# Performance work log

Measured on AMD Instinct MI355X. Metric: run time of the kernel, lower is better.

Reference implementation:

```python
import jax, jax.numpy as jnp
import numpy as np

P = 16          # patch size
D = 256         # embed dim (complex channels)
L = 2           # depth (num blocks)
NE = 4          # num experts
FF = 1024       # ffn hidden = expand * D
B, T, C, IH, IW = 1, 8, 4, 256, 256
HP, WP = IH // P, IW // P


def setup_inputs():
    key = jax.random.key(0)
    ks = iter(jax.random.split(key, 40))
    r = lambda shape, s=0.02: jax.random.normal(next(ks), shape, jnp.float32) * s
    sD = 1.0 / np.sqrt(D)
    return {
        'x': jax.random.normal(next(ks), (B, T, C, IH, IW), jnp.float32),
        'dt': jax.random.uniform(next(ks), (B, T), jnp.float32, 0.1, 1.0),
        'Wenc': r((C * P * P, 2 * D)),
        'benc': jnp.zeros((2 * D,), jnp.float32),
        'Wdec': r((2 * D, C * P * P)),
        'bdec': jnp.zeros((C * P * P,), jnp.float32),
        'ln_sp_w': jnp.ones((L, 2 * D), jnp.float32),
        'ln_sp_b': jnp.zeros((L, 2 * D), jnp.float32),
        'conv_w': r((L, 2 * D, 2 * D, 3, 3)),
        'conv_b': jnp.zeros((L, 2 * D), jnp.float32),
        'E_re': r((L, D, D), sD), 'E_im': r((L, D, D), sD),
        'Ed_re': r((L, D, D), sD), 'Ed_im': r((L, D, D), sD),
        'Ws_re': r((L, D, D), sD), 'Ws_im': r((L, D, D), sD),
        'Wg': r((L, 2 * D, D)),
        'bg': jnp.zeros((L, D), jnp.float32),
        'lam_re': r((L, D), 1.0), 'lam_im': r((L, D), 1.0),
        'ln_t_w': jnp.ones((L, 2 * D), jnp.float32),
        'ln_t_b': jnp.zeros((L, 2 * D), jnp.float32),
        'Wr': r((L, 2 * D, NE)),
        'W1': r((L, NE, 2 * D, FF)),
        'W2': r((L, NE, FF, 2 * D)),
    }


def _ln(x, w, b):
    m = x.mean(-1, keepdims=True)
    v = ((x - m) ** 2).mean(-1, keepdims=True)
    return (x - m) * jax.lax.rsqrt(v + 1e-5) * w + b


def _block(z, h_prev, flux_prev, dt, bp):
    (ln_sp_w, ln_sp_b, conv_w, conv_b, E_re, E_im, Ed_re, Ed_im,
     Ws_re, Ws_im, Wg, bg, lam_re, lam_im, ln_t_w, ln_t_b, Wr, W1, W2) = bp
    Bq, Tq, Dq, H, W = z.shape
    # --- spatial process: LN + conv on concat(real, imag), complex residual ---
    zf = z.reshape(Bq * Tq, Dq, H, W)
    zr = jnp.concatenate([zf.real, zf.imag], axis=1)
    zn = _ln(zr.transpose(0, 2, 3, 1), ln_sp_w, ln_sp_b).transpose(0, 3, 1, 2)
    zs = jax.lax.conv_general_dilated(zn, conv_w, (1, 1), 'SAME',
                                      dimension_numbers=('NCHW', 'OIHW', 'NCHW'))
    zs = zs + conv_b[None, :, None, None]
    re, im = jnp.split(zs, 2, axis=1)
    x = (zf + (re + 1j * im)).reshape(Bq, Tq, Dq, H, W)
    # --- eigen-basis encode ---
    Eb = E_re + 1j * E_im
    x_eigen = jnp.einsum('btdhw,de->bthwe', x, Eb)   # [B,T,H,W,D] complex
    x_mean = x_eigen.mean(axis=(2, 3))               # [B,T,D] complex
    # --- sequential gated flux recurrence over T ---
    Ws = Ws_re + 1j * Ws_im
    def step(flux, xm):
        source = xm @ Ws
        feat = jnp.concatenate([xm.real, xm.imag], -1)
        gate = jax.nn.sigmoid(feat @ Wg + bg)        # real [B,D]
        new_flux = gate * flux + (1.0 - gate) * source
        return new_flux, (new_flux, source, gate)
    _, (flux_seq, source_seq, gate_seq) = jax.lax.scan(step, flux_prev, x_mean.transpose(1, 0, 2))
    flux_seq = flux_seq.transpose(1, 0, 2)
    source_seq = source_seq.transpose(1, 0, 2)
    gate_seq = gate_seq.transpose(1, 0, 2)
    g = gate_seq[:, :, None, None, :]
    forcing = x_eigen * g + source_seq[:, :, None, None, :] * (1.0 - g)
    # --- transition operators ---
    lam = -(jax.nn.softplus(lam_re) + 1e-2) + 1j * lam_im        # [D]
    op_decay = jnp.exp(lam[None, None, :] * dt[:, :, None])      # [B,T,D] complex
    op_forcing = (op_decay - 1.0) / lam
    a = jnp.broadcast_to(op_decay[:, :, None, None, :], forcing.shape)
    u = forcing * op_forcing[:, :, None, None, :]
    # --- parallel linear scan h_t = a_t * h_{t-1} + u_t along T ---
    def comb(c1, c2):
        a1, u1 = c1
        a2, u2 = c2
        return a1 * a2, u1 * a2 + u2
    _, h = jax.lax.associative_scan(comb, (a, u), axis=1)
    # as written in source: h_prev contribution is h_prev * op_decay at every t
    h = h + h_prev.reshape(Bq, 1, H, W, Dq) * a
    last_h = h[:, -1].reshape(Bq * H * W, 1, Dq)
    last_flux = flux_seq[:, -1]
    # --- eigen decode + temporal LN + MoE FFN ---
    Ed = Ed_re + 1j * Ed_im
    x_out = jnp.einsum('bthwe,ed->btdhw', h, Ed)
    xf = x_out.reshape(Bq * Tq, Dq, H, W)
    xr = jnp.concatenate([xf.real, xf.imag], axis=1)
    xn = _ln(xr.transpose(0, 2, 3, 1), ln_t_w, ln_t_b)           # [BT,H,W,2D]
    tok = xn.reshape(-1, 2 * Dq)
    probs = jax.nn.softmax(tok @ Wr, axis=-1)                    # [N,E]
    hid = jax.nn.gelu(jnp.einsum('nd,edf->nef', tok, W1))
    y = jnp.einsum('nef,efd,ne->nd', hid, W2, probs)             # [N,2D]
    xc = xn[..., :Dq] + 1j * xn[..., Dq:]
    delta = (y[..., :Dq] + 1j * y[..., Dq:]).reshape(Bq * Tq, H, W, Dq)
    x_cplx = (xc + delta).reshape(Bq, Tq, H, W, Dq).transpose(0, 1, 4, 2, 3)
    return x + x_cplx, last_h, last_flux


def _forward(x, dt, Wenc, benc, Wdec, bdec, ln_sp_w, ln_sp_b, conv_w, conv_b,
             E_re, E_im, Ed_re, Ed_im, Ws_re, Ws_im, Wg, bg, lam_re, lam_im,
             ln_t_w, ln_t_b, Wr, W1, W2):
    # encoder: patchify + linear -> complex latent [B,T,D,HP,WP]
    xp = x.reshape(B, T, C, HP, P, WP, P).transpose(0, 1, 3, 5, 2, 4, 6)
    xp = xp.reshape(B, T, HP, WP, C * P * P)
    ze = xp @ Wenc + benc                                        # [B,T,HP,WP,2D]
    z = (ze[..., :D] + 1j * ze[..., D:]).transpose(0, 1, 4, 2, 3)
    h_prev = jnp.zeros((B * HP * WP, 1, D), jnp.complex64)
    flux_prev = jnp.zeros((B, D), jnp.complex64)
    bparams = (ln_sp_w, ln_sp_b, conv_w, conv_b, E_re, E_im, Ed_re, Ed_im,
               Ws_re, Ws_im, Wg, bg, lam_re, lam_im, ln_t_w, ln_t_b, Wr, W1, W2)
    for i in range(L):
        bp = tuple(p[i] for p in bparams)
        z, h_prev, flux_prev = _block(z, h_prev, flux_prev, dt, bp)
    # decoder: linear + unpatchify (real output)
    zr = jnp.concatenate([z.real, z.imag], axis=2).transpose(0, 1, 3, 4, 2)
    yo = zr @ Wdec + bdec                                        # [B,T,HP,WP,C*P*P]
    out = yo.reshape(B, T, HP, WP, C, P, P).transpose(0, 1, 4, 2, 5, 3, 6)
    return out.reshape(B, T, C, IH, IW)


def reference(x, dt, Wenc, benc, Wdec, bdec, ln_sp_w, ln_sp_b, conv_w, conv_b,
              E_re, E_im, Ed_re, Ed_im, Ws_re, Ws_im, Wg, bg, lam_re, lam_im,
              ln_t_w, ln_t_b, Wr, W1, W2):
    return _forward(x, dt, Wenc, benc, Wdec, bdec, ln_sp_w, ln_sp_b, conv_w, conv_b,
                    E_re, E_im, Ed_re, Ed_im, Ws_re, Ws_im, Wg, bg, lam_re, lam_im,
                    ln_t_w, ln_t_b, Wr, W1, W2)
```

## Files before the change

### kernel.cpp

```cpp
#include <hip/hip_runtime.h>
#include <hip/hip_bf16.h>


#define TOKS 2048

typedef __bf16 bf16;
typedef __attribute__((ext_vector_type(8))) __bf16 bf16x8;
typedef __attribute__((ext_vector_type(4))) __bf16 bf16x4;
typedef __attribute__((ext_vector_type(4))) float f32x4;

enum GMode { EENC = 0, ECONV, ESQ, EMOE1, EMOE2, EDEC };

template <int MODE>
__global__ __launch_bounds__(256) void mgemm_k(
    const bf16* __restrict__ A, const bf16* __restrict__ Bt,
    const float* __restrict__ bias, float* __restrict__ C, int K, int N) {
  __shared__ __align__(16) bf16 As[64 * 40];
  __shared__ __align__(16) bf16 Bs[64 * 40];
  const int tid = threadIdx.x;
  const int bm = blockIdx.x * 64, bn = blockIdx.y * 64;
  const int lane = tid & 63, w = tid >> 6;
  const int wm = (w & 1) * 32, wn = (w >> 1) * 32;
  const int quad = lane >> 4, l16 = lane & 15;
  const int srow = tid >> 2, sko = (tid & 3) << 3;

  f32x4 acc[2][2] = {};
  const int kiter = K / 32;

  auto loadA = [&](int kt) -> bf16x8 {
    return *(const bf16x8*)&A[(size_t)(bm + srow) * K + kt * 32 + sko];
  };
  auto loadB = [&](int kt) -> bf16x8 {
    return *(const bf16x8*)&Bt[(size_t)(bn + srow) * K + kt * 32 + sko];
  };

  bf16x8 pa = loadA(0), pb = loadB(0);
  for (int kt = 0; kt < kiter; kt++) {
    *(bf16x8*)&As[srow * 40 + sko] = pa;
    *(bf16x8*)&Bs[srow * 40 + sko] = pb;
    __syncthreads();
    if (kt + 1 < kiter) {
      pa = loadA(kt + 1);
      pb = loadB(kt + 1);
    }
    const bf16x8 a0 = *(const bf16x8*)&As[(wm + l16) * 40 + quad * 8];
    const bf16x8 a1 = *(const bf16x8*)&As[(wm + 16 + l16) * 40 + quad * 8];
    const bf16x8 b0 = *(const bf16x8*)&Bs[(wn + l16) * 40 + quad * 8];
    const bf16x8 b1 = *(const bf16x8*)&Bs[(wn + 16 + l16) * 40 + quad * 8];
    acc[0][0] = __builtin_amdgcn_mfma_f32_16x16x32_bf16(a0, b0, acc[0][0], 0, 0, 0);
    acc[0][1] = __builtin_amdgcn_mfma_f32_16x16x32_bf16(a0, b1, acc[0][1], 0, 0, 0);
    acc[1][0] = __builtin_amdgcn_mfma_f32_16x16x32_bf16(a1, b0, acc[1][0], 0, 0, 0);
    acc[1][1] = __builtin_amdgcn_mfma_f32_16x16x32_bf16(a1, b1, acc[1][1], 0, 0, 0);
    __syncthreads();
  }

#pragma unroll
  for (int i = 0; i < 2; i++) {
#pragma unroll
    for (int j = 0; j < 2; j++) {
#pragma unroll
      for (int r = 0; r < 4; r++) {
        const int gm = bm + wm + i * 16 + quad * 4 + r;
        const int gn = bn + wn + j * 16 + l16;
        const float v = acc[i][j][r];
        if constexpr (MODE == EENC) {
          C[(size_t)gm * 512 + gn] = v + bias[gn];
        } else if constexpr (MODE == ESQ) {
          C[(size_t)gm * 512 + gn] = v;
        } else {
          const int t = gm >> 8, hp = (gm >> 4) & 15, wp = gm & 15;
          const int c = gn >> 8, ph = (gn >> 4) & 15, pw = gn & 15;
          C[(size_t)(((t * 4 + c) * 256 + hp * 16 + ph) << 8) + wp * 16 + pw] =
              v + bias[gn];
        }
      }
    }
  }
}

template <int MODE, int SPLIT>
__global__ __launch_bounds__(256) void mgemm2_k(
    const bf16* __restrict__ A, const bf16* __restrict__ Bt,
    const float* __restrict__ scalev, bf16* __restrict__ C16,
    float* __restrict__ Cpart, int K, int N) {
  __shared__ __align__(16) bf16 As[128 * 40];
  __shared__ __align__(16) bf16 Bs[128 * 40];
  const int tid = threadIdx.x;
  const int bm = blockIdx.x * 128, bn = blockIdx.y * 128;
  const int lane = tid & 63, w = tid >> 6;
  const int wm = (w & 1) * 64, wn = (w >> 1) * 64;
  const int quad = lane >> 4, l16 = lane & 15;
  const int srow = tid >> 1, sko = (tid & 1) << 4;

  const int kbase = (SPLIT > 1) ? blockIdx.z * (K / SPLIT) : 0;
  const int kiter = K / (32 * SPLIT);
  if constexpr (MODE == EMOE1) Bt += (size_t)blockIdx.z * 524288;

  f32x4 acc[4][4] = {};

  int cv_t = 0, cv_h = 0, cv_w = 0;
  if constexpr (MODE == ECONV) {
    const int gm = bm + srow;
    cv_t = gm >> 8;
    cv_h = (gm >> 4) & 15;
    cv_w = gm & 15;
  }

  auto loadA = [&](int kt, int half) -> bf16x8 {
    const int gk = kbase + kt * 32 + sko + half * 8;
    if constexpr (MODE == ECONV) {
      const int s = gk >> 9, ci = gk & 511;
      const int kh = s / 3, kw = s - kh * 3;
      const int hh = cv_h + kh - 1, ww = cv_w + kw - 1;
      if (hh >= 0 && hh < 16 && ww >= 0 && ww < 16)
        return *(const bf16x8*)&A[(size_t)(((cv_t << 8) + hh * 16 + ww) << 9) +
                                  ci];
      bf16x8 zz;
#pragma unroll
      for (int q = 0; q < 8; q++) zz[q] = (bf16)0.0f;
      return zz;
    } else {
      return *(const bf16x8*)&A[(size_t)(bm + srow) * K + gk];
    }
  };
  auto loadB = [&](int kt, int half) -> bf16x8 {
    return *(const bf16x8*)&Bt[(size_t)(bn + srow) * K + kbase + kt * 32 + sko +
                               half * 8];
  };

  bf16x8 pa0 = loadA(0, 0), pa1 = loadA(0, 1);
  bf16x8 pb0 = loadB(0, 0), pb1 = loadB(0, 1);
  for (int kt = 0; kt < kiter; kt++) {
    *(bf16x8*)&As[srow * 40 + sko] = pa0;
    *(bf16x8*)&As[srow * 40 + sko + 8] = pa1;
    *(bf16x8*)&Bs[srow * 40 + sko] = pb0;
    *(bf16x8*)&Bs[srow * 40 + sko + 8] = pb1;
    __syncthreads();
    if (kt + 1 < kiter) {
      pa0 = loadA(kt + 1, 0);
      pa1 = loadA(kt + 1, 1);
      pb0 = loadB(kt + 1, 0);
      pb1 = loadB(kt + 1, 1);
    }
    bf16x8 af[4], bfr[4];
#pragma unroll
    for (int i = 0; i < 4; i++)
      af[i] = *(const bf16x8*)&As[(wm + i * 16 + l16) * 40 + quad * 8];
#pragma unroll
    for (int j = 0; j < 4; j++)
      bfr[j] = *(const bf16x8*)&Bs[(wn + j * 16 + l16) * 40 + quad * 8];
#pragma unroll
    for (int i = 0; i < 4; i++)
#pragma unroll
      for (int j = 0; j < 4; j++)
        acc[i][j] =
            __builtin_amdgcn_mfma_f32_16x16x32_bf16(af[i], bfr[j], acc[i][j], 0, 0, 0);
    __syncthreads();
  }

#pragma unroll
  for (int i = 0; i < 4; i++) {
#pragma unroll
    for (int j = 0; j < 4; j++) {
#pragma unroll
      for (int r = 0; r < 4; r++) {
        const int gm = bm + wm + i * 16 + quad * 4 + r;
        const int gn = bn + wn + j * 16 + l16;
        const float v = acc[i][j][r];
        if constexpr (SPLIT > 1) {
          Cpart[(size_t)blockIdx.z * 1048576 + (size_t)gm * 512 + gn] = v;
        } else {
          const float t = 0.7978845608028654f * (v + 0.044715f * v * v * v);
          const float g = 0.5f * v * (1.f + tanhf(t));
          const float p = scalev[gm * 4 + blockIdx.z];
          C16[(size_t)gm * 4096 + blockIdx.z * 1024 + gn] = (bf16)(p * g);
        }
      }
    }
  }
}

__global__ __launch_bounds__(256) void conv_ep_k(
    const float* __restrict__ parts, const float* __restrict__ bias,
    const float* __restrict__ resid, float* __restrict__ xb,
    bf16* __restrict__ xb16) {
  const int i4 = (blockIdx.x * 256 + threadIdx.x) << 2;
  const int c = i4 & 511;
  const float4 p0 = *(const float4*)&parts[i4];
  const float4 p1 = *(const float4*)&parts[1048576 + i4];
  const float4 p2 = *(const float4*)&parts[2097152 + i4];
  const float4 p3 = *(const float4*)&parts[3145728 + i4];
  const float4 bi = *(const float4*)&bias[c];
  const float4 rz = *(const float4*)&resid[i4];
  float4 o;
  o.x = p0.x + p1.x + p2.x + p3.x + bi.x + rz.x;
  o.y = p0.y + p1.y + p2.y + p3.y + bi.y + rz.y;
  o.z = p0.z + p1.z + p2.z + p3.z + bi.z + rz.z;
  o.w = p0.w + p1.w + p2.w + p3.w + bi.w + rz.w;
  *(float4*)&xb[i4] = o;
  bf16x4 o16 = {(bf16)o.x, (bf16)o.y, (bf16)o.z, (bf16)o.w};
  *(bf16x4*)&xb16[i4] = o16;
}

__global__ __launch_bounds__(256) void addf_k(const float* __restrict__ xb,
                                              const float* __restrict__ zn,
                                              const float* __restrict__ parts,
                                              float* __restrict__ z,
                                              bf16* __restrict__ z16) {
  const int i4 = (blockIdx.x * 256 + threadIdx.x) << 2;
  const float4 a = *(const float4*)&xb[i4];
  const float4 b = *(const float4*)&zn[i4];
  const float4 p0 = *(const float4*)&parts[i4];
  const float4 p1 = *(const float4*)&parts[1048576 + i4];
  const float4 p2 = *(const float4*)&parts[2097152 + i4];
  const float4 p3 = *(const float4*)&parts[3145728 + i4];
  float4 o;
  o.x = a.x + b.x + p0.x + p1.x + p2.x + p3.x;
  o.y = a.y + b.y + p0.y + p1.y + p2.y + p3.y;
  o.z = a.z + b.z + p0.z + p1.z + p2.z + p3.z;
  o.w = a.w + b.w + p0.w + p1.w + p2.w + p3.w;
  *(float4*)&z[i4] = o;
  bf16x4 o16 = {(bf16)o.x, (bf16)o.y, (bf16)o.z, (bf16)o.w};
  *(bf16x4*)&z16[i4] = o16;
}

template <bool DO_PROBS>
__global__ __launch_bounds__(256) void ln_k(
    const float* __restrict__ in, const float* __restrict__ w,
    const float* __restrict__ b, const float* __restrict__ Wr,
    float* __restrict__ out, bf16* __restrict__ out16,
    float* __restrict__ probs) {
  const int wv = threadIdx.x >> 6, lane = threadIdx.x & 63;
  const int n = (blockIdx.x << 2) + wv;
  const float* row = in + (size_t)n * 512;
  float v[8];
  float s = 0.f, s2 = 0.f;
#pragma unroll
  for (int i = 0; i < 8; i++) {
    const float x = row[(i << 6) + lane];
    v[i] = x;
    s += x;
    s2 += x * x;
  }
#pragma unroll
  for (int off = 32; off > 0; off >>= 1) {
    s += __shfl_down(s, off);
    s2 += __shfl_down(s2, off);
  }
  s = __shfl(s, 0);
  s2 = __shfl(s2, 0);
  const float m = s * (1.f / 512.f);
  const float var = s2 * (1.f / 512.f) - m * m;
  const float r = rsqrtf(var + 1e-5f);
  float a0 = 0.f, a1 = 0.f, a2 = 0.f, a3 = 0.f;
#pragma unroll
  for (int i = 0; i < 8; i++) {
    const int c = (i << 6) + lane;
    const float o = (v[i] - m) * r * w[c] + b[c];
    out[(size_t)n * 512 + c] = o;
    out16[(size_t)n * 512 + c] = (bf16)o;
    if constexpr (DO_PROBS) {
      a0 += o * Wr[c * 4 + 0];
      a1 += o * Wr[c * 4 + 1];
      a2 += o * Wr[c * 4 + 2];
      a3 += o * Wr[c * 4 + 3];
    }
  }
  if constexpr (DO_PROBS) {
#pragma unroll
    for (int off = 32; off > 0; off >>= 1) {
      a0 += __shfl_down(a0, off);
      a1 += __shfl_down(a1, off);
      a2 += __shfl_down(a2, off);
      a3 += __shfl_down(a3, off);
    }
    if (lane == 0) {
      const float mx = fmaxf(fmaxf(a0, a1), fmaxf(a2, a3));
      const float e0 = expf(a0 - mx), e1 = expf(a1 - mx), e2 = expf(a2 - mx),
                  e3 = expf(a3 - mx);
      const float inv = 1.f / (e0 + e1 + e2 + e3);
      probs[n * 4 + 0] = e0 * inv;
      probs[n * 4 + 1] = e1 * inv;
      probs[n * 4 + 2] = e2 * inv;
      probs[n * 4 + 3] = e3 * inv;
    }
  }
}

__global__ __launch_bounds__(256) void cvt_all_k(
    const float* __restrict__ x, const float* __restrict__ Wenc,
    const float* __restrict__ Wdec, const float* __restrict__ W1,
    const float* __restrict__ W2, const float* __restrict__ E_re,
    const float* __restrict__ E_im, const float* __restrict__ Ed_re,
    const float* __restrict__ Ed_im, const float* __restrict__ conv_w,
    bf16* __restrict__ Ae, bf16* __restrict__ WencT, bf16* __restrict__ WdecT,
    bf16* __restrict__ W1T, bf16* __restrict__ W2Tc, bf16* __restrict__ MEt,
    bf16* __restrict__ convBt) {
  __shared__ float tile[32][33];
  const int tid = threadIdx.x;
  int b = blockIdx.x;
  const int tx = tid & 31, ty = tid >> 5;
  auto tpose = [&](const float* src, bf16* dst, int K, int N, int dstride,
                   int k0, int n0) {
#pragma unroll
    for (int r = 0; r < 4; r++)
      tile[ty + 8 * r][tx] = src[(size_t)(k0 + ty + 8 * r) * N + n0 + tx];
    __syncthreads();
#pragma unroll
    for (int r = 0; r < 4; r++)
      dst[(size_t)(n0 + ty + 8 * r) * dstride + k0 + tx] =
          (bf16)tile[tx][ty + 8 * r];
  };
  if (b < 1024) {
    const int id = b * 256 + tid;
    const int n = id >> 7;
    const int kc = (id & 127) << 3;
    const int t = n >> 8, hp = (n >> 4) & 15, wp = n & 15;
    const int c = kc >> 8, ph = (kc >> 4) & 15, pw = kc & 15;
    const float* src =
        &x[(size_t)(((t * 4 + c) * 256 + hp * 16 + ph) << 8) + wp * 16 + pw];
    const float4 v0 = *(const float4*)src;
    const float4 v1 = *(const float4*)(src + 4);
    bf16* d = &Ae[(size_t)n * 1024 + kc];
    d[0] = (bf16)v0.x; d[1] = (bf16)v0.y; d[2] = (bf16)v0.z; d[3] = (bf16)v0.w;
    d[4] = (bf16)v1.x; d[5] = (bf16)v1.y; d[6] = (bf16)v1.z; d[7] = (bf16)v1.w;
    return;
  }
  b -= 1024;
  if (b < 512) {
    tpose(Wenc, WencT, 1024, 512, 1024, (b & 31) * 32, (b >> 5) * 32);
    return;
  }
  b -= 512;
  if (b < 512) {
    tpose(Wdec, WdecT, 512, 1024, 512, (b & 15) * 32, (b >> 4) * 32);
    return;
  }
  b -= 512;
  if (b < 4096) {
    const int z = b >> 9, rem = b & 511;
    tpose(W1 + (size_t)z * 524288, W1T + (size_t)z * 524288, 512, 1024, 512,
          (rem & 15) * 32, (rem >> 4) * 32);
    return;
  }
  b -= 4096;
  if (b < 4096) {
    const int z = b >> 9, rem = b & 511;
    const int l = z >> 2, e = z & 3;
    tpose(W2 + (size_t)z * 524288, W2Tc + (size_t)l * 2097152 + e * 1024, 1024,
          512, 4096, (rem & 31) * 32, (rem >> 5) * 32);
    return;
  }
  b -= 4096;
  if (b < 4096) {
    const int z = b >> 10;
    const int l = z >> 1, which = z & 1;
    const float* Er = (which ? Ed_re : E_re) + l * 65536;
    const float* Ei = (which ? Ed_im : E_im) + l * 65536;
    bf16* dst = MEt + (size_t)z * 262144;
    const int idx = (b & 1023) * 256 + tid;
    const int j = idx >> 9, k = idx & 511;
    const int kk = k & 255, jj = j & 255;
    const float er = Er[kk * 256 + jj], ei = Ei[kk * 256 + jj];
    const float v = (k < 256) ? ((j < 256) ? er : ei) : ((j < 256) ? -ei : er);
    dst[idx] = (bf16)v;
    return;
  }
  b -= 4096;
  {
    const int z = b / 2304;
    const int rem = b - z * 2304;
    const float* src = conv_w + (size_t)z * 2359296;
    bf16* d = convBt + (size_t)z * 2359296;
    const int idx = (rem * 256 + tid) << 2;
    const int co = idx / 4608;
    const int r2 = idx - co * 4608;
    const int s = r2 >> 9, ci = r2 & 511;
    bf16x4 o;
#pragma unroll
    for (int q = 0; q < 4; q++)
      o[q] = (bf16)src[(size_t)(co * 512 + ci + q) * 9 + s];
    *(bf16x4*)&d[idx] = o;
  }
}

__global__ __launch_bounds__(256) void srcgate_k(
    const float* __restrict__ xe, const float* __restrict__ Wsr,
    const float* __restrict__ Wsi, const float* __restrict__ Wg,
    const float* __restrict__ bg, float* __restrict__ srcs,
    float* __restrict__ gts) {
  const int t = blockIdx.x, part = blockIdx.y, d = threadIdx.x;
  __shared__ float sxm[512];
  for (int c = d; c < 512; c += 256) {
    const float* col = xe + (size_t)(t << 8) * 512 + c;
    float s0 = 0.f, s1 = 0.f, s2 = 0.f, s3 = 0.f;
    for (int p = 0; p < 256; p += 4) {
      s0 += col[(size_t)(p + 0) * 512];
      s1 += col[(size_t)(p + 1) * 512];
      s2 += col[(size_t)(p + 2) * 512];
      s3 += col[(size_t)(p + 3) * 512];
    }
    sxm[c] = ((s0 + s1) + (s2 + s3)) * (1.f / 256.f);
  }
  __syncthreads();
  if (part == 0) {
    float s0 = 0.f, s1 = 0.f, s2 = 0.f, s3 = 0.f;
#pragma unroll 4
    for (int e = 0; e < 256; e += 4) {
      s0 += sxm[e + 0] * Wsr[(e + 0) * 256 + d] - sxm[256 + e + 0] * Wsi[(e + 0) * 256 + d];
      s1 += sxm[e + 1] * Wsr[(e + 1) * 256 + d] - sxm[256 + e + 1] * Wsi[(e + 1) * 256 + d];
      s2 += sxm[e + 2] * Wsr[(e + 2) * 256 + d] - sxm[256 + e + 2] * Wsi[(e + 2) * 256 + d];
      s3 += sxm[e + 3] * Wsr[(e + 3) * 256 + d] - sxm[256 + e + 3] * Wsi[(e + 3) * 256 + d];
    }
    srcs[t * 512 + d] = (s0 + s1) + (s2 + s3);
  } else if (part == 1) {
    float s0 = 0.f, s1 = 0.f, s2 = 0.f, s3 = 0.f;
#pragma unroll 4
    for (int e = 0; e < 256; e += 4) {
      s0 += sxm[e + 0] * Wsi[(e + 0) * 256 + d] + sxm[256 + e + 0] * Wsr[(e + 0) * 256 + d];
      s1 += sxm[e + 1] * Wsi[(e + 1) * 256 + d] + sxm[256 + e + 1] * Wsr[(e + 1) * 256 + d];
      s2 += sxm[e + 2] * Wsi[(e + 2) * 256 + d] + sxm[256 + e + 2] * Wsr[(e + 2) * 256 + d];
      s3 += sxm[e + 3] * Wsi[(e + 3) * 256 + d] + sxm[256 + e + 3] * Wsr[(e + 3) * 256 + d];
    }
    srcs[t * 512 + 256 + d] = (s0 + s1) + (s2 + s3);
  } else {
    float s0 = 0.f, s1 = 0.f, s2 = 0.f, s3 = 0.f;
#pragma unroll 4
    for (int c = 0; c < 512; c += 4) {
      s0 += sxm[c + 0] * Wg[(c + 0) * 256 + d];
      s1 += sxm[c + 1] * Wg[(c + 1) * 256 + d];
      s2 += sxm[c + 2] * Wg[(c + 2) * 256 + d];
      s3 += sxm[c + 3] * Wg[(c + 3) * 256 + d];
    }
    const float ga = (s0 + s1) + (s2 + s3) + bg[d];
    gts[t * 256 + d] = 1.f / (1.f + expf(-ga));
  }
}

template <bool FIRST>
__global__ __launch_bounds__(256) void time_scan_k(
    const float* __restrict__ xe, const float* __restrict__ gts,
    const float* __restrict__ srcs, const float* __restrict__ lamre,
    const float* __restrict__ lamim, const float* __restrict__ dt,
    bf16* __restrict__ hout16, float* __restrict__ hprev) {
  const int d = threadIdx.x;
  const int p = blockIdx.x;
  const float lr0 = lamre[d];
  const float sp = (lr0 > 20.f) ? lr0 : log1pf(expf(lr0));
  const float lre = -(sp + 0.01f);
  const float lim = lamim[d];
  const float den = lre * lre + lim * lim;
  float ar[8], ai[8], ofr[8], ofi[8];
#pragma unroll
  for (int t = 0; t < 8; t++) {
    const float dtv = dt[t];
    const float er = expf(lre * dtv);
    const float odr = er * cosf(lim * dtv);
    const float odi = er * sinf(lim * dtv);
    ar[t] = odr;
    ai[t] = odi;
    const float nr = odr - 1.f, ni = odi;
    ofr[t] = (nr * lre + ni * lim) / den;
    ofi[t] = (ni * lre - nr * lim) / den;
  }
  float hr = 0.f, hi = 0.f;
  float hpr = 0.f, hpi = 0.f;
  if constexpr (!FIRST) {
    hpr = hprev[p * 512 + d];
    hpi = hprev[p * 512 + 256 + d];
  }
  float o7r = 0.f, o7i = 0.f;
#pragma unroll
  for (int t = 0; t < 8; t++) {
    const size_t base = (size_t)((t << 8) + p) * 512;
    const float xr = xe[base + d], xi = xe[base + 256 + d];
    const float g = gts[t * 256 + d];
    const float sr = srcs[t * 512 + d], si = srcs[t * 512 + 256 + d];
    const float fr = xr * g + sr * (1.f - g);
    const float fi = xi * g + si * (1.f - g);
    const float ur = fr * ofr[t] - fi * ofi[t];
    const float ui = fr * ofi[t] + fi * ofr[t];
    const float nhr = ur + ar[t] * hr - ai[t] * hi;
    const float nhi = ui + ar[t] * hi + ai[t] * hr;
    hr = nhr;
    hi = nhi;
    const float outr = hr + ar[t] * hpr - ai[t] * hpi;
    const float outi = hi + ar[t] * hpi + ai[t] * hpr;
    hout16[base + d] = (bf16)outr;
    hout16[base + 256 + d] = (bf16)outi;
    if (t == 7) {
      o7r = outr;
      o7i = outi;
    }
  }
  hprev[p * 512 + d] = o7r;
  hprev[p * 512 + 256 + d] = o7i;
}

extern "C" void kernel_launch(void* const* d_in, const int* in_sizes, int n_in,
                              void* d_out, int out_size, void* d_ws,
                              size_t ws_size, hipStream_t stream) {
  const float* x_in = (const float*)d_in[0];
  const float* dt = (const float*)d_in[1];
  const float* Wenc = (const float*)d_in[2];
  const float* benc = (const float*)d_in[3];
  const float* Wdec = (const float*)d_in[4];
  const float* bdec = (const float*)d_in[5];
  const float* ln_sp_w = (const float*)d_in[6];
  const float* ln_sp_b = (const float*)d_in[7];
  const float* conv_w = (const float*)d_in[8];
  const float* conv_b = (const float*)d_in[9];
  const float* E_re = (const float*)d_in[10];
  const float* E_im = (const float*)d_in[11];
  const float* Ed_re = (const float*)d_in[12];
  const float* Ed_im = (const float*)d_in[13];
  const float* Ws_re = (const float*)d_in[14];
  const float* Ws_im = (const float*)d_in[15];
  const float* Wg = (const float*)d_in[16];
  const float* bg = (const float*)d_in[17];
  const float* lam_re = (const float*)d_in[18];
  const float* lam_im = (const float*)d_in[19];
  const float* ln_t_w = (const float*)d_in[20];
  const float* ln_t_b = (const float*)d_in[21];
  const float* Wr = (const float*)d_in[22];
  const float* W1 = (const float*)d_in[23];
  const float* W2 = (const float*)d_in[24];
  float* out = (float*)d_out;

  float* ws = (float*)d_ws;
  size_t off = 0;
  auto allocf = [&](size_t n) {
    float* p = ws + off;
    off += n;
    return p;
  };
  auto allocb = [&](size_t n) {
    bf16* p = (bf16*)(ws + off);
    off += n / 2;
    return p;
  };
  float* z = allocf((size_t)TOKS * 512);
  float* zn = allocf((size_t)TOKS * 512);
  float* xb = allocf((size_t)TOKS * 512);
  float* xe = allocf((size_t)TOKS * 512);
  float* parts = allocf((size_t)4 * TOKS * 512);
  float* hprev = allocf(256 * 512);
  float* srcs = allocf(8 * 512);
  float* gts = allocf(8 * 256);
  float* probs = allocf((size_t)TOKS * 4);
  bf16* zn16 = allocb((size_t)TOKS * 512);
  bf16* xb16 = allocb((size_t)TOKS * 512);
  bf16* z16 = allocb((size_t)TOKS * 512);
  bf16* hb16 = allocb((size_t)TOKS * 512);
  bf16* hid16 = allocb((size_t)TOKS * 4096);
  bf16* Aenc16 = allocb((size_t)TOKS * 1024);
  bf16* WencT = allocb((size_t)512 * 1024);
  bf16* WdecT = allocb((size_t)1024 * 512);
  bf16* MEt = allocb((size_t)4 * 512 * 512);
  bf16* convBt = allocb((size_t)2 * 512 * 4608);
  bf16* W1T = allocb((size_t)8 * 1024 * 512);
  bf16* W2Tc = allocb((size_t)2 * 512 * 4096);

  cvt_all_k<<<18944, 256, 0, stream>>>(x_in, Wenc, Wdec, W1, W2, E_re, E_im,
                                       Ed_re, Ed_im, conv_w, Aenc16, WencT,
                                       WdecT, W1T, W2Tc, MEt, convBt);

  mgemm_k<EENC><<<dim3(32, 8), 256, 0, stream>>>(Aenc16, WencT, benc, z, 1024,
                                                 512);

  for (int l = 0; l < 2; l++) {
    ln_k<false><<<512, 256, 0, stream>>>(z, ln_sp_w + l * 512,
                                         ln_sp_b + l * 512, nullptr, zn, zn16,
                                         nullptr);
    mgemm2_k<ECONV, 4><<<dim3(16, 4, 4), 256, 0, stream>>>(
        zn16, convBt + (size_t)l * 512 * 4608, nullptr, nullptr, parts, 4608,
        512);
    conv_ep_k<<<1024, 256, 0, stream>>>(parts, conv_b + l * 512, z, xb, xb16);
    mgemm_k<ESQ><<<dim3(32, 8), 256, 0, stream>>>(
        xb16, MEt + (size_t)(l * 2) * 262144, nullptr, xe, 512, 512);
    srcgate_k<<<dim3(8, 3), 256, 0, stream>>>(xe, Ws_re + l * 65536,
                                              Ws_im + l * 65536,
                                              Wg + l * 131072, bg + l * 256,
                                              srcs, gts);
    if (l == 0)
      time_scan_k<true><<<256, 256, 0, stream>>>(
          xe, gts, srcs, lam_re, lam_im, dt, hb16, hprev);
    else
      time_scan_k<false><<<256, 256, 0, stream>>>(
          xe, gts, srcs, lam_re + 256, lam_im + 256, dt, hb16, hprev);
    mgemm_k<ESQ><<<dim3(32, 8), 256, 0, stream>>>(
        hb16, MEt + (size_t)(l * 2 + 1) * 262144, nullptr, xe, 512, 512);
    ln_k<true><<<512, 256, 0, stream>>>(xe, ln_t_w + l * 512, ln_t_b + l * 512,
                                        Wr + l * 2048, zn, zn16, probs);
    mgemm2_k<EMOE1, 1><<<dim3(16, 8, 4), 256, 0, stream>>>(
        zn16, W1T + (size_t)l * 2097152, probs, hid16, nullptr, 512, 1024);
    mgemm2_k<EMOE2, 4><<<dim3(16, 4, 4), 256, 0, stream>>>(
        hid16, W2Tc + (size_t)l * 2097152, nullptr, nullptr, parts, 4096, 512);
    addf_k<<<1024, 256, 0, stream>>>(xb, zn, parts, z, z16);
  }

  mgemm_k<EDEC><<<dim3(32, 16), 256, 0, stream>>>(z16, WdecT, bdec, out, 512,
                                                  1024);
}
```

Baseline: 495.1 us.

## Unify GEMMs on 64x64 tiles, split-K small GEMMs, fuse LN into combine kernels

```diff
diff --git a/kernel.cpp b/kernel.cpp
--- a/kernel.cpp
+++ b/kernel.cpp
@@ -3,6 +3,7 @@
 
 
 #define TOKS 2048
+#define PSLICE 1048576
 
 typedef __bf16 bf16;
 typedef __attribute__((ext_vector_type(8))) __bf16 bf16x8;
@@ -11,10 +12,12 @@
 
 enum GMode { EENC = 0, ECONV, ESQ, EMOE1, EMOE2, EDEC };
 
-template <int MODE>
+template <int MODE, int SPLIT>
 __global__ __launch_bounds__(256) void mgemm_k(
     const bf16* __restrict__ A, const bf16* __restrict__ Bt,
-    const float* __restrict__ bias, float* __restrict__ C, int K, int N) {
+    const float* __restrict__ bias, const float* __restrict__ scalev,
+    float* __restrict__ C, bf16* __restrict__ C16, float* __restrict__ Cpart,
+    int K, int N) {
   __shared__ __align__(16) bf16 As[64 * 40];
   __shared__ __align__(16) bf16 Bs[64 * 40];
   const int tid = threadIdx.x;
@@ -24,14 +27,39 @@
   const int quad = lane >> 4, l16 = lane & 15;
   const int srow = tid >> 2, sko = (tid & 3) << 3;
 
+  const int kbase = (SPLIT > 1) ? blockIdx.z * (K / SPLIT) : 0;
+  const int kiter = K / (32 * SPLIT);
+  if constexpr (MODE == EMOE1) Bt += (size_t)blockIdx.z * 524288;
+
   f32x4 acc[2][2] = {};
-  const int kiter = K / 32;
+
+  int cv_t = 0, cv_h = 0, cv_w = 0;
+  if constexpr (MODE == ECONV) {
+    const int gm = bm + srow;
+    cv_t = gm >> 8;
+    cv_h = (gm >> 4) & 15;
+    cv_w = gm & 15;
+  }
 
   auto loadA = [&](int kt) -> bf16x8 {
-    return *(const bf16x8*)&A[(size_t)(bm + srow) * K + kt * 32 + sko];
+    const int gk = kbase + kt * 32 + sko;
+    if constexpr (MODE == ECONV) {
+      const int s = gk >> 9, ci = gk & 511;
+      const int kh = s / 3, kw = s - kh * 3;
+      const int hh = cv_h + kh - 1, ww = cv_w + kw - 1;
+      if (hh >= 0 && hh < 16 && ww >= 0 && ww < 16)
+        return *(const bf16x8*)&A[(size_t)(((cv_t << 8) + hh * 16 + ww) << 9) +
+                                  ci];
+      bf16x8 zz;
+#pragma unroll
+      for (int q = 0; q < 8; q++) zz[q] = (bf16)0.0f;
+      return zz;
+    } else {
+      return *(const bf16x8*)&A[(size_t)(bm + srow) * K + gk];
+    }
   };
   auto loadB = [&](int kt) -> bf16x8 {
-    return *(const bf16x8*)&Bt[(size_t)(bn + srow) * K + kt * 32 + sko];
+    return *(const bf16x8*)&Bt[(size_t)(bn + srow) * K + kbase + kt * 32 + sko];
   };
 
   bf16x8 pa = loadA(0), pb = loadB(0);
@@ -63,10 +91,13 @@
         const int gm = bm + wm + i * 16 + quad * 4 + r;
         const int gn = bn + wn + j * 16 + l16;
         const float v = acc[i][j][r];
-        if constexpr (MODE == EENC) {
-          C[(size_t)gm * 512 + gn] = v + bias[gn];
-        } else if constexpr (MODE == ESQ) {
-          C[(size_t)gm * 512 + gn] = v;
+        if constexpr (SPLIT > 1) {
+          Cpart[(size_t)blockIdx.z * PSLICE + (size_t)gm * 512 + gn] = v;
+        } else if constexpr (MODE == EMOE1) {
+          const float t = 0.7978845608028654f * (v + 0.044715f * v * v * v);
+          const float g = 0.5f * v * (1.f + tanhf(t));
+          const float p = scalev[gm * 4 + blockIdx.z];
+          C16[(size_t)gm * 4096 + blockIdx.z * 1024 + gn] = (bf16)(p * g);
         } else {
           const int t = gm >> 8, hp = (gm >> 4) & 15, wp = gm & 15;
           const int c = gn >> 8, ph = (gn >> 4) & 15, pw = gn & 15;
@@ -78,108 +109,6 @@
   }
 }
 
-template <int MODE, int SPLIT>
-__global__ __launch_bounds__(256) void mgemm2_k(
-    const bf16* __restrict__ A, const bf16* __restrict__ Bt,
-    const float* __restrict__ scalev, bf16* __restrict__ C16,
-    float* __restrict__ Cpart, int K, int N) {
-  __shared__ __align__(16) bf16 As[128 * 40];
-  __shared__ __align__(16) bf16 Bs[128 * 40];
-  const int tid = threadIdx.x;
-  const int bm = blockIdx.x * 128, bn = blockIdx.y * 128;
-  const int lane = tid & 63, w = tid >> 6;
-  const int wm = (w & 1) * 64, wn = (w >> 1) * 64;
-  const int quad = lane >> 4, l16 = lane & 15;
-  const int srow = tid >> 1, sko = (tid & 1) << 4;
-
-  const int kbase = (SPLIT > 1) ? blockIdx.z * (K / SPLIT) : 0;
-  const int kiter = K / (32 * SPLIT);
-  if constexpr (MODE == EMOE1) Bt += (size_t)blockIdx.z * 524288;
-
-  f32x4 acc[4][4] = {};
-
-  int cv_t = 0, cv_h = 0, cv_w = 0;
-  if constexpr (MODE == ECONV) {
-    const int gm = bm + srow;
-    cv_t = gm >> 8;
-    cv_h = (gm >> 4) & 15;
-    cv_w = gm & 15;
-  }
-
-  auto loadA = [&](int kt, int half) -> bf16x8 {
-    const int gk = kbase + kt * 32 + sko + half * 8;
-    if constexpr (MODE == ECONV) {
-      const int s = gk >> 9, ci = gk & 511;
-      const int kh = s / 3, kw = s - kh * 3;
-      const int hh = cv_h + kh - 1, ww = cv_w + kw - 1;
-      if (hh >= 0 && hh < 16 && ww >= 0 && ww < 16)
-        return *(const bf16x8*)&A[(size_t)(((cv_t << 8) + hh * 16 + ww) << 9) +
-                                  ci];
-      bf16x8 zz;
-#pragma unroll
-      for (int q = 0; q < 8; q++) zz[q] = (bf16)0.0f;
-      return zz;
-    } else {
-      return *(const bf16x8*)&A[(size_t)(bm + srow) * K + gk];
-    }
-  };
-  auto loadB = [&](int kt, int half) -> bf16x8 {
-    return *(const bf16x8*)&Bt[(size_t)(bn + srow) * K + kbase + kt * 32 + sko +
-                               half * 8];
-  };
-
-  bf16x8 pa0 = loadA(0, 0), pa1 = loadA(0, 1);
-  bf16x8 pb0 = loadB(0, 0), pb1 = loadB(0, 1);
-  for (int kt = 0; kt < kiter; kt++) {
-    *(bf16x8*)&As[srow * 40 + sko] = pa0;
-    *(bf16x8*)&As[srow * 40 + sko + 8] = pa1;
-    *(bf16x8*)&Bs[srow * 40 + sko] = pb0;
-    *(bf16x8*)&Bs[srow * 40 + sko + 8] = pb1;
-    __syncthreads();
-    if (kt + 1 < kiter) {
-      pa0 = loadA(kt + 1, 0);
-      pa1 = loadA(kt + 1, 1);
-      pb0 = loadB(kt + 1, 0);
-      pb1 = loadB(kt + 1, 1);
-    }
-    bf16x8 af[4], bfr[4];
-#pragma unroll
-    for (int i = 0; i < 4; i++)
-      af[i] = *(const bf16x8*)&As[(wm + i * 16 + l16) * 40 + quad * 8];
-#pragma unroll
-    for (int j = 0; j < 4; j++)
-      bfr[j] = *(const bf16x8*)&Bs[(wn + j * 16 + l16) * 40 + quad * 8];
-#pragma unroll
-    for (int i = 0; i < 4; i++)
-#pragma unroll
-      for (int j = 0; j < 4; j++)
-        acc[i][j] =
-            __builtin_amdgcn_mfma_f32_16x16x32_bf16(af[i], bfr[j], acc[i][j], 0, 0, 0);
-    __syncthreads();
-  }
-
-#pragma unroll
-  for (int i = 0; i < 4; i++) {
-#pragma unroll
-    for (int j = 0; j < 4; j++) {
-#pragma unroll
-      for (int r = 0; r < 4; r++) {
-        const int gm = bm + wm + i * 16 + quad * 4 + r;
-        const int gn = bn + wn + j * 16 + l16;
-        const float v = acc[i][j][r];
-        if constexpr (SPLIT > 1) {
-          Cpart[(size_t)blockIdx.z * 1048576 + (size_t)gm * 512 + gn] = v;
-        } else {
-          const float t = 0.7978845608028654f * (v + 0.044715f * v * v * v);
-          const float g = 0.5f * v * (1.f + tanhf(t));
-          const float p = scalev[gm * 4 + blockIdx.z];
-          C16[(size_t)gm * 4096 + blockIdx.z * 1024 + gn] = (bf16)(p * g);
-        }
-      }
-    }
-  }
-}
-
 __global__ __launch_bounds__(256) void conv_ep_k(
     const float* __restrict__ parts, const float* __restrict__ bias,
     const float* __restrict__ resid, float* __restrict__ xb,
@@ -187,9 +116,9 @@
   const int i4 = (blockIdx.x * 256 + threadIdx.x) << 2;
   const int c = i4 & 511;
   const float4 p0 = *(const float4*)&parts[i4];
-  const float4 p1 = *(const float4*)&parts[1048576 + i4];
-  const float4 p2 = *(const float4*)&parts[2097152 + i4];
-  const float4 p3 = *(const float4*)&parts[3145728 + i4];
+  const float4 p1 = *(const float4*)&parts[PSLICE + i4];
+  const float4 p2 = *(const float4*)&parts[2 * PSLICE + i4];
+  const float4 p3 = *(const float4*)&parts[3 * PSLICE + i4];
   const float4 bi = *(const float4*)&bias[c];
   const float4 rz = *(const float4*)&resid[i4];
   float4 o;
@@ -202,42 +131,22 @@
   *(bf16x4*)&xb16[i4] = o16;
 }
 
-__global__ __launch_bounds__(256) void addf_k(const float* __restrict__ xb,
-                                              const float* __restrict__ zn,
-                                              const float* __restrict__ parts,
-                                              float* __restrict__ z,
-                                              bf16* __restrict__ z16) {
-  const int i4 = (blockIdx.x * 256 + threadIdx.x) << 2;
-  const float4 a = *(const float4*)&xb[i4];
-  const float4 b = *(const float4*)&zn[i4];
-  const float4 p0 = *(const float4*)&parts[i4];
-  const float4 p1 = *(const float4*)&parts[1048576 + i4];
-  const float4 p2 = *(const float4*)&parts[2097152 + i4];
-  const float4 p3 = *(const float4*)&parts[3145728 + i4];
-  float4 o;
-  o.x = a.x + b.x + p0.x + p1.x + p2.x + p3.x;
-  o.y = a.y + b.y + p0.y + p1.y + p2.y + p3.y;
-  o.z = a.z + b.z + p0.z + p1.z + p2.z + p3.z;
-  o.w = a.w + b.w + p0.w + p1.w + p2.w + p3.w;
-  *(float4*)&z[i4] = o;
-  bf16x4 o16 = {(bf16)o.x, (bf16)o.y, (bf16)o.z, (bf16)o.w};
-  *(bf16x4*)&z16[i4] = o16;
-}
-
-template <bool DO_PROBS>
-__global__ __launch_bounds__(256) void ln_k(
-    const float* __restrict__ in, const float* __restrict__ w,
-    const float* __restrict__ b, const float* __restrict__ Wr,
-    float* __restrict__ out, bf16* __restrict__ out16,
+template <bool ENC>
+__global__ __launch_bounds__(256) void ln_comb_k(
+    const float* __restrict__ parts, const float* __restrict__ bias,
+    const float* __restrict__ w, const float* __restrict__ b,
+    const float* __restrict__ Wr, float* __restrict__ zout,
+    float* __restrict__ out32, bf16* __restrict__ out16,
     float* __restrict__ probs) {
   const int wv = threadIdx.x >> 6, lane = threadIdx.x & 63;
   const int n = (blockIdx.x << 2) + wv;
-  const float* row = in + (size_t)n * 512;
   float v[8];
   float s = 0.f, s2 = 0.f;
 #pragma unroll
   for (int i = 0; i < 8; i++) {
-    const float x = row[(i << 6) + lane];
+    const int c = (i << 6) + lane;
+    float x = parts[(size_t)n * 512 + c] + parts[PSLICE + (size_t)n * 512 + c];
+    if constexpr (ENC) x += bias[c];
     v[i] = x;
     s += x;
     s2 += x * x;
@@ -257,16 +166,18 @@
   for (int i = 0; i < 8; i++) {
     const int c = (i << 6) + lane;
     const float o = (v[i] - m) * r * w[c] + b[c];
-    out[(size_t)n * 512 + c] = o;
-    out16[(size_t)n * 512 + c] = (bf16)o;
-    if constexpr (DO_PROBS) {
+    if constexpr (ENC) {
+      zout[(size_t)n * 512 + c] = v[i];
+    } else {
+      out32[(size_t)n * 512 + c] = o;
       a0 += o * Wr[c * 4 + 0];
       a1 += o * Wr[c * 4 + 1];
       a2 += o * Wr[c * 4 + 2];
       a3 += o * Wr[c * 4 + 3];
     }
-  }
-  if constexpr (DO_PROBS) {
+    out16[(size_t)n * 512 + c] = (bf16)o;
+  }
+  if constexpr (!ENC) {
 #pragma unroll
     for (int off = 32; off > 0; off >>= 1) {
       a0 += __shfl_down(a0, off);
@@ -287,6 +198,50 @@
   }
 }
 
+template <bool DO_LN>
+__global__ __launch_bounds__(256) void addf2_k(
+    const float* __restrict__ xb, const float* __restrict__ xn,
+    const float* __restrict__ parts, const float* __restrict__ w,
+    const float* __restrict__ b, float* __restrict__ zout,
+    bf16* __restrict__ out16) {
+  const int wv = threadIdx.x >> 6, lane = threadIdx.x & 63;
+  const int n = (blockIdx.x << 2) + wv;
+  float v[8];
+  float s = 0.f, s2 = 0.f;
+#pragma unroll
+  for (int i = 0; i < 8; i++) {
+    const size_t idx = (size_t)n * 512 + (i << 6) + lane;
+    const float x = xb[idx] + xn[idx] + parts[idx] + parts[PSLICE + idx] +
+                    parts[2 * PSLICE + idx] + parts[3 * PSLICE + idx];
+    v[i] = x;
+    s += x;
+    s2 += x * x;
+  }
+  if constexpr (!DO_LN) {
+#pragma unroll
+    for (int i = 0; i < 8; i++)
+      out16[(size_t)n * 512 + (i << 6) + lane] = (bf16)v[i];
+    return;
+  }
+#pragma unroll
+  for (int off = 32; off > 0; off >>= 1) {
+    s += __shfl_down(s, off);
+    s2 += __shfl_down(s2, off);
+  }
+  s = __shfl(s, 0);
+  s2 = __shfl(s2, 0);
+  const float m = s * (1.f / 512.f);
+  const float var = s2 * (1.f / 512.f) - m * m;
+  const float r = rsqrtf(var + 1e-5f);
+#pragma unroll
+  for (int i = 0; i < 8; i++) {
+    const int c = (i << 6) + lane;
+    const float x = v[i];
+    zout[(size_t)n * 512 + c] = x;
+    out16[(size_t)n * 512 + c] = (bf16)((x - m) * r * w[c] + b[c]);
+  }
+}
+
 __global__ __launch_bounds__(256) void cvt_all_k(
     const float* __restrict__ x, const float* __restrict__ Wenc,
     const float* __restrict__ Wdec, const float* __restrict__ W1,
@@ -296,12 +251,13 @@
     bf16* __restrict__ Ae, bf16* __restrict__ WencT, bf16* __restrict__ WdecT,
     bf16* __restrict__ W1T, bf16* __restrict__ W2Tc, bf16* __restrict__ MEt,
     bf16* __restrict__ convBt) {
-  __shared__ float tile[32][33];
+  __shared__ float smem[4608];
+  float(*tile)[33] = (float(*)[33])smem;
   const int tid = threadIdx.x;
   int b = blockIdx.x;
   const int tx = tid & 31, ty = tid >> 5;
-  auto tpose = [&](const float* src, bf16* dst, int K, int N, int dstride,
-                   int k0, int n0) {
+  auto tpose = [&](const float* src, bf16* dst, int N, int dstride, int k0,
+                   int n0) {
 #pragma unroll
     for (int r = 0; r < 4; r++)
       tile[ty + 8 * r][tx] = src[(size_t)(k0 + ty + 8 * r) * N + n0 + tx];
@@ -328,18 +284,18 @@
   }
   b -= 1024;
   if (b < 512) {
-    tpose(Wenc, WencT, 1024, 512, 1024, (b & 31) * 32, (b >> 5) * 32);
+    tpose(Wenc, WencT, 512, 1024, (b & 31) * 32, (b >> 5) * 32);
     return;
   }
   b -= 512;
   if (b < 512) {
-    tpose(Wdec, WdecT, 512, 1024, 512, (b & 15) * 32, (b >> 4) * 32);
+    tpose(Wdec, WdecT, 1024, 512, (b & 15) * 32, (b >> 4) * 32);
     return;
   }
   b -= 512;
   if (b < 4096) {
     const int z = b >> 9, rem = b & 511;
-    tpose(W1 + (size_t)z * 524288, W1T + (size_t)z * 524288, 512, 1024, 512,
+    tpose(W1 + (size_t)z * 524288, W1T + (size_t)z * 524288, 1024, 512,
           (rem & 15) * 32, (rem >> 4) * 32);
     return;
   }
@@ -347,8 +303,8 @@
   if (b < 4096) {
     const int z = b >> 9, rem = b & 511;
     const int l = z >> 2, e = z & 3;
-    tpose(W2 + (size_t)z * 524288, W2Tc + (size_t)l * 2097152 + e * 1024, 1024,
-          512, 4096, (rem & 31) * 32, (rem >> 5) * 32);
+    tpose(W2 + (size_t)z * 524288, W2Tc + (size_t)l * 2097152 + e * 1024, 512,
+          4096, (rem & 31) * 32, (rem >> 5) * 32);
     return;
   }
   b -= 4096;
@@ -368,39 +324,34 @@
   }
   b -= 4096;
   {
-    const int z = b / 2304;
-    const int rem = b - z * 2304;
-    const float* src = conv_w + (size_t)z * 2359296;
-    bf16* d = convBt + (size_t)z * 2359296;
-    const int idx = (rem * 256 + tid) << 2;
-    const int co = idx / 4608;
-    const int r2 = idx - co * 4608;
-    const int s = r2 >> 9, ci = r2 & 511;
-    bf16x4 o;
-#pragma unroll
-    for (int q = 0; q < 4; q++)
-      o[q] = (bf16)src[(size_t)(co * 512 + ci + q) * 9 + s];
-    *(bf16x4*)&d[idx] = o;
+    const int l = b >> 9, co = b & 511;
+    const float* src = conv_w + (size_t)l * 2359296 + (size_t)co * 4608;
+    bf16* d = convBt + (size_t)l * 2359296 + (size_t)co * 4608;
+    for (int i = tid; i < 4608; i += 256) smem[i] = src[i];
+    __syncthreads();
+    for (int o = tid; o < 4608; o += 256) {
+      const int s = o >> 9, ci = o & 511;
+      d[o] = (bf16)smem[ci * 9 + s];
+    }
   }
 }
 
 __global__ __launch_bounds__(256) void srcgate_k(
-    const float* __restrict__ xe, const float* __restrict__ Wsr,
+    const float* __restrict__ parts, const float* __restrict__ Wsr,
     const float* __restrict__ Wsi, const float* __restrict__ Wg,
     const float* __restrict__ bg, float* __restrict__ srcs,
     float* __restrict__ gts) {
   const int t = blockIdx.x, part = blockIdx.y, d = threadIdx.x;
   __shared__ float sxm[512];
   for (int c = d; c < 512; c += 256) {
-    const float* col = xe + (size_t)(t << 8) * 512 + c;
-    float s0 = 0.f, s1 = 0.f, s2 = 0.f, s3 = 0.f;
-    for (int p = 0; p < 256; p += 4) {
-      s0 += col[(size_t)(p + 0) * 512];
-      s1 += col[(size_t)(p + 1) * 512];
-      s2 += col[(size_t)(p + 2) * 512];
-      s3 += col[(size_t)(p + 3) * 512];
-    }
-    sxm[c] = ((s0 + s1) + (s2 + s3)) * (1.f / 256.f);
+    const float* col0 = parts + (size_t)(t << 8) * 512 + c;
+    const float* col1 = col0 + PSLICE;
+    float s0 = 0.f, s1 = 0.f;
+    for (int p = 0; p < 256; p += 2) {
+      s0 += col0[(size_t)p * 512] + col1[(size_t)p * 512];
+      s1 += col0[(size_t)(p + 1) * 512] + col1[(size_t)(p + 1) * 512];
+    }
+    sxm[c] = (s0 + s1) * (1.f / 256.f);
   }
   __syncthreads();
   if (part == 0) {
@@ -439,7 +390,7 @@
 
 template <bool FIRST>
 __global__ __launch_bounds__(256) void time_scan_k(
-    const float* __restrict__ xe, const float* __restrict__ gts,
+    const float* __restrict__ parts, const float* __restrict__ gts,
     const float* __restrict__ srcs, const float* __restrict__ lamre,
     const float* __restrict__ lamim, const float* __restrict__ dt,
     bf16* __restrict__ hout16, float* __restrict__ hprev) {
@@ -473,7 +424,8 @@
 #pragma unroll
   for (int t = 0; t < 8; t++) {
     const size_t base = (size_t)((t << 8) + p) * 512;
-    const float xr = xe[base + d], xi = xe[base + 256 + d];
+    const float xr = parts[base + d] + parts[PSLICE + base + d];
+    const float xi = parts[base + 256 + d] + parts[PSLICE + base + 256 + d];
     const float g = gts[t * 256 + d];
     const float sr = srcs[t * 512 + d], si = srcs[t * 512 + 256 + d];
     const float fr = xr * g + sr * (1.f - g);
@@ -540,15 +492,15 @@
     return p;
   };
   float* z = allocf((size_t)TOKS * 512);
-  float* zn = allocf((size_t)TOKS * 512);
+  float* xn = allocf((size_t)TOKS * 512);
   float* xb = allocf((size_t)TOKS * 512);
-  float* xe = allocf((size_t)TOKS * 512);
-  float* parts = allocf((size_t)4 * TOKS * 512);
+  float* parts = allocf((size_t)4 * PSLICE);
   float* hprev = allocf(256 * 512);
   float* srcs = allocf(8 * 512);
   float* gts = allocf(8 * 256);
   float* probs = allocf((size_t)TOKS * 4);
-  bf16* zn16 = allocb((size_t)TOKS * 512);
+  bf16* znsp16 = allocb((size_t)TOKS * 512);
+  bf16* xn16 = allocb((size_t)TOKS * 512);
   bf16* xb16 = allocb((size_t)TOKS * 512);
   bf16* z16 = allocb((size_t)TOKS * 512);
   bf16* hb16 = allocb((size_t)TOKS * 512);
@@ -561,44 +513,55 @@
   bf16* W1T = allocb((size_t)8 * 1024 * 512);
   bf16* W2Tc = allocb((size_t)2 * 512 * 4096);
 
-  cvt_all_k<<<18944, 256, 0, stream>>>(x_in, Wenc, Wdec, W1, W2, E_re, E_im,
+  cvt_all_k<<<15360, 256, 0, stream>>>(x_in, Wenc, Wdec, W1, W2, E_re, E_im,
                                        Ed_re, Ed_im, conv_w, Aenc16, WencT,
                                        WdecT, W1T, W2Tc, MEt, convBt);
 
-  mgemm_k<EENC><<<dim3(32, 8), 256, 0, stream>>>(Aenc16, WencT, benc, z, 1024,
-                                                 512);
+  mgemm_k<EENC, 2><<<dim3(32, 8, 2), 256, 0, stream>>>(
+      Aenc16, WencT, nullptr, nullptr, nullptr, nullptr, parts, 1024, 512);
+  ln_comb_k<true><<<512, 256, 0, stream>>>(parts, benc, ln_sp_w, ln_sp_b,
+                                           nullptr, z, nullptr, znsp16,
+                                           nullptr);
 
   for (int l = 0; l < 2; l++) {
-    ln_k<false><<<512, 256, 0, stream>>>(z, ln_sp_w + l * 512,
-                                         ln_sp_b + l * 512, nullptr, zn, zn16,
-                                         nullptr);
-    mgemm2_k<ECONV, 4><<<dim3(16, 4, 4), 256, 0, stream>>>(
-        zn16, convBt + (size_t)l * 512 * 4608, nullptr, nullptr, parts, 4608,
-        512);
+    mgemm_k<ECONV, 4><<<dim3(32, 8, 4), 256, 0, stream>>>(
+        znsp16, convBt + (size_t)l * 2359296, nullptr, nullptr, nullptr,
+        nullptr, parts, 4608, 512);
     conv_ep_k<<<1024, 256, 0, stream>>>(parts, conv_b + l * 512, z, xb, xb16);
-    mgemm_k<ESQ><<<dim3(32, 8), 256, 0, stream>>>(
-        xb16, MEt + (size_t)(l * 2) * 262144, nullptr, xe, 512, 512);
-    srcgate_k<<<dim3(8, 3), 256, 0, stream>>>(xe, Ws_re + l * 65536,
+    mgemm_k<ESQ, 2><<<dim3(32, 8, 2), 256, 0, stream>>>(
+        xb16, MEt + (size_t)(l * 2) * 262144, nullptr, nullptr, nullptr,
+        nullptr, parts, 512, 512);
+    srcgate_k<<<dim3(8, 3), 256, 0, stream>>>(parts, Ws_re + l * 65536,
                                               Ws_im + l * 65536,
                                               Wg + l * 131072, bg + l * 256,
                                               srcs, gts);
     if (l == 0)
-      time_scan_k<true><<<256, 256, 0, stream>>>(
-          xe, gts, srcs, lam_re, lam_im, dt, hb16, hprev);
+      time_scan_k<true><<<256, 256, 0, stream>>>(parts, gts, srcs, lam_re,
+                                                 lam_im, dt, hb16, hprev);
     else
-      time_scan_k<false><<<256, 256, 0, stream>>>(
-          xe, gts, srcs, lam_re + 256, lam_im + 256, dt, hb16, hprev);
-    mgemm_k<ESQ><<<dim3(32, 8), 256, 0, stream>>>(
-        hb16, MEt + (size_t)(l * 2 + 1) * 262144, nullptr, xe, 512, 512);
-    ln_k<true><<<512, 256, 0, stream>>>(xe, ln_t_w + l * 512, ln_t_b + l * 512,
-                                        Wr + l * 2048, zn, zn16, probs);
-    mgemm2_k<EMOE1, 1><<<dim3(16, 8, 4), 256, 0, stream>>>(
-        zn16, W1T + (size_t)l * 2097152, probs, hid16, nullptr, 512, 1024);
-    mgemm2_k<EMOE2, 4><<<dim3(16, 4, 4), 256, 0, stream>>>(
-        hid16, W2Tc + (size_t)l * 2097152, nullptr, nullptr, parts, 4096, 512);
-    addf_k<<<1024, 256, 0, stream>>>(xb, zn, parts, z, z16);
-  }
-
-  mgemm_k<EDEC><<<dim3(32, 16), 256, 0, stream>>>(z16, WdecT, bdec, out, 512,
-                                                  1024);
-}
+      time_scan_k<false><<<256, 256, 0, stream>>>(parts, gts, srcs,
+                                                  lam_re + 256, lam_im + 256,
+                                                  dt, hb16, hprev);
+    mgemm_k<ESQ, 2><<<dim3(32, 8, 2), 256, 0, stream>>>(
+        hb16, MEt + (size_t)(l * 2 + 1) * 262144, nullptr, nullptr, nullptr,
+        nullptr, parts, 512, 512);
+    ln_comb_k<false><<<512, 256, 0, stream>>>(parts, nullptr, ln_t_w + l * 512,
+                                              ln_t_b + l * 512, Wr + l * 2048,
+                                              nullptr, xn, xn16, probs);
+    mgemm_k<EMOE1, 1><<<dim3(32, 16, 4), 256, 0, stream>>>(
+        xn16, W1T + (size_t)l * 2097152, nullptr, probs, nullptr, hid16,
+        nullptr, 512, 1024);
+    mgemm_k<EMOE2, 4><<<dim3(32, 8, 4), 256, 0, stream>>>(
+        hid16, W2Tc + (size_t)l * 2097152, nullptr, nullptr, nullptr, nullptr,
+        parts, 4096, 512);
+    if (l == 0)
+      addf2_k<true><<<512, 256, 0, stream>>>(xb, xn, parts, ln_sp_w + 512,
+                                             ln_sp_b + 512, z, znsp16);
+    else
+      addf2_k<false><<<512, 256, 0, stream>>>(xb, xn, parts, nullptr, nullptr,
+                                              nullptr, z16);
+  }
+
+  mgemm_k<EDEC, 1><<<dim3(32, 16), 256, 0, stream>>>(
+      z16, WdecT, bdec, nullptr, out, nullptr, nullptr, 512, 1024);
+}
```

Result: faster. 478.5 us (-3.4%).
